# Performance work log

Hardware: AMD Instinct MI355X
Metric: run time of the kernel (lower is better)

Reference implementation:

```python
import jax, jax.numpy as jnp
import numpy as np

OUT, IN = 8192, 8192
GROUP = 128
N_GROUPS = IN // GROUP
BATCH = 64


def dequant_int4(packed, scales):
    # packed: [OUT, IN//2] int32 bytes in [0,256); two 4-bit codes per byte
    low = packed & 0xF            # first element of each pair
    high = (packed >> 4) & 0xF    # second element
    q = jnp.stack([low, high], axis=-1).reshape(OUT, IN)  # interleaved nibbles
    # symmetric grouped dequant: w = (q - 8) * scale, scale per [row, group]
    qg = q.reshape(OUT, N_GROUPS, GROUP).astype(scales.dtype)
    w = (qg - 8.0) * scales[:, :, None]
    return w.reshape(OUT, IN)


def setup_inputs() -> dict:
    key = jax.random.key(0)
    k1, k2, k3 = jax.random.split(key, 3)
    x = jax.random.normal(k1, (BATCH, IN), dtype=jnp.float32)
    packed = jax.random.randint(k2, (OUT, IN // 2), 0, 256, dtype=jnp.int32)
    scales = jax.random.uniform(k3, (OUT, N_GROUPS), dtype=jnp.float32)
    return {"x": x, "packed": packed, "scales": scales}


def reference(x, packed, scales):
    # Dequantize int4 weights then dense matmul (F.linear, no bias)
    w = dequant_int4(packed, scales)        # [OUT, IN]
    return jnp.einsum('bi,oi->bo', x, w)    # [BATCH, OUT]
```

## Files before the change

kernel.cpp:

```cpp
#include <hip/hip_runtime.h>
#include <hip/hip_bf16.h>
#include <stdint.h>

#define OUTN   8192
#define INN    8192
#define NGRP   64
#define BATCHN 64
#define BN     64
#define BK     128
#define KSPLIT 8
#define KCHUNK (INN / KSPLIT)
#define NITER  (KCHUNK / BK)
#define OSZ    (BATCHN * OUTN)

typedef __attribute__((ext_vector_type(8))) short bf16x8;
typedef __attribute__((ext_vector_type(4))) float f32x4;
typedef __attribute__((ext_vector_type(4))) unsigned int u32x4;

__device__ __forceinline__ unsigned short f2bf(float f) {
  __hip_bfloat16 h = __float2bfloat16(f);
  return __builtin_bit_cast(unsigned short, h);
}
__device__ __forceinline__ float bf2f(unsigned short h) {
  unsigned int u = ((unsigned int)h) << 16;
  return __builtin_bit_cast(float, u);
}

__global__ void qlin_prep(const float* __restrict__ x, float* __restrict__ xsum) {
  const int b = blockIdx.x;
  const int t = threadIdx.x;
  const float* xrow = x + (size_t)b * INN + t * 32;
  float s = 0.0f;
#pragma unroll
  for (int i = 0; i < 8; ++i) {
    float4 v = *(const float4*)(xrow + i * 4);
    s += bf2f(f2bf(v.x)) + bf2f(f2bf(v.y)) + bf2f(f2bf(v.z)) + bf2f(f2bf(v.w));
  }
  __shared__ float part[256];
  part[t] = s;
  __syncthreads();
  if (t < NGRP) {
    float g = part[4 * t] + part[4 * t + 1] + part[4 * t + 2] + part[4 * t + 3];
    xsum[t * BATCHN + b] = g;
  }
}

#define PKS 17
#define XTS 136

__global__ __launch_bounds__(256, 4) void qlin_main(
    const float* __restrict__ x, const int* __restrict__ packed,
    const float* __restrict__ scales, const float* __restrict__ xsum,
    float* __restrict__ out, float* __restrict__ part) {
  const int bx    = blockIdx.x;
  const int ks    = bx & (KSPLIT - 1);
  const int ntile = bx >> 3;
  const int o0    = ntile * BN;
  const int g0    = ks * NITER;

  const int t    = threadIdx.x;
  const int lane = t & 63;
  const int w    = t >> 6;
  const int l15  = lane & 15;
  const int quad = lane >> 4;

  __shared__ __align__(16) unsigned int   pk_c[BN * PKS];
  __shared__ __align__(16) unsigned short xt[BATCHN * XTS];
  __shared__ __align__(16) float          st[BN][9];
  __shared__ __align__(16) float          xs[NITER][BATCHN];

#pragma unroll
  for (int i = 0; i < 2; ++i) {
    int v = t * 2 + i;
    int ol = v >> 3, gl = v & 7;
    st[ol][gl] = scales[(size_t)(o0 + ol) * NGRP + g0 + gl];
    int gl2 = v >> 6, b2 = v & 63;
    xs[gl2][b2] = xsum[(g0 + gl2) * BATCHN + b2];
  }

  int4   pkr[4];
  float4 xr[8];

  const int prow = t >> 4, pcol = t & 15;
  const int xrow = t >> 5, xcol = t & 31;

  auto load_tile = [&](int i) {
    const int kk2 = ks * (KCHUNK / 2) + i * (BK / 2);
    const int* pbase = packed + (size_t)(o0 + prow) * (INN / 2) + kk2 + pcol * 4;
#pragma unroll
    for (int j = 0; j < 4; ++j)
      pkr[j] = *(const int4*)(pbase + (size_t)(16 * j) * (INN / 2));
    const int kk = ks * KCHUNK + i * BK;
    const float* xbase = x + (size_t)xrow * INN + kk + xcol * 4;
#pragma unroll
    for (int j = 0; j < 8; ++j)
      xr[j] = *(const float4*)(xbase + (size_t)(8 * j) * INN);
  };

  auto store_tile = [&]() {
#pragma unroll
    for (int j = 0; j < 4; ++j) {
      unsigned int c = (unsigned)pkr[j].x | ((unsigned)pkr[j].y << 8) |
                       ((unsigned)pkr[j].z << 16) | ((unsigned)pkr[j].w << 24);
      pk_c[(prow + 16 * j) * PKS + pcol] = c;
    }
#pragma unroll
    for (int j = 0; j < 8; ++j) {
      ushort4 h;
      h.x = f2bf(xr[j].x); h.y = f2bf(xr[j].y);
      h.z = f2bf(xr[j].z); h.w = f2bf(xr[j].w);
      *(ushort4*)&xt[(xrow + 8 * j) * XTS + xcol * 4] = h;
    }
  };

  f32x4 facc[4];
#pragma unroll
  for (int mt = 0; mt < 4; ++mt) facc[mt] = (f32x4){0.f, 0.f, 0.f, 0.f};

  load_tile(0);

  for (int i = 0; i < NITER; ++i) {
    __syncthreads();
    store_tile();
    if (i + 1 < NITER) load_tile(i + 1);
    __syncthreads();

    f32x4 gacc[4];
#pragma unroll
    for (int mt = 0; mt < 4; ++mt) gacc[mt] = (f32x4){0.f, 0.f, 0.f, 0.f};

#pragma unroll
    for (int kq = 0; kq < 4; ++kq) {
      bf16x8 af[4];
#pragma unroll
      for (int mt = 0; mt < 4; ++mt)
        af[mt] = *(const bf16x8*)&xt[(mt * 16 + l15) * XTS + kq * 32 + quad * 8];

      unsigned int c = pk_c[(w * 16 + l15) * PKS + kq * 4 + quad];
      u32x4 bw;
      bw.x = 0x43004300u | (c & 0xFu) | ((c & 0xF0u) << 12);
      bw.y = 0x43004300u | ((c >> 8) & 0xFu) | (((c >> 8) & 0xF0u) << 12);
      bw.z = 0x43004300u | ((c >> 16) & 0xFu) | (((c >> 16) & 0xF0u) << 12);
      bw.w = 0x43004300u | ((c >> 24) & 0xFu) | (((c >> 24) & 0xF0u) << 12);
      bf16x8 bfv = __builtin_bit_cast(bf16x8, bw);

#pragma unroll
      for (int mt = 0; mt < 4; ++mt)
        gacc[mt] = __builtin_amdgcn_mfma_f32_16x16x32_bf16(af[mt], bfv, gacc[mt], 0, 0, 0);
    }

    float s0 = st[w * 16 + l15][i];
#pragma unroll
    for (int mt = 0; mt < 4; ++mt) {
      f32x4 xv = *(const f32x4*)&xs[i][mt * 16 + quad * 4];
#pragma unroll
      for (int r = 0; r < 4; ++r)
        facc[mt][r] += s0 * (gacc[mt][r] - 136.0f * xv[r]);
    }
  }

  const int obase = o0 + w * 16 + l15;
  if (part) {
    float* pb = part + (size_t)ks * OSZ;
#pragma unroll
    for (int mt = 0; mt < 4; ++mt)
#pragma unroll
      for (int r = 0; r < 4; ++r) {
        int m = mt * 16 + quad * 4 + r;
        pb[(size_t)m * OUTN + obase] = facc[mt][r];
      }
  } else {
#pragma unroll
    for (int mt = 0; mt < 4; ++mt)
#pragma unroll
      for (int r = 0; r < 4; ++r) {
        int m = mt * 16 + quad * 4 + r;
        atomicAdd(&out[(size_t)m * OUTN + obase], facc[mt][r]);
      }
  }
}

__global__ void qlin_reduce(const float* __restrict__ part, float* __restrict__ out) {
  const size_t i = ((size_t)blockIdx.x * 256 + threadIdx.x) * 4;
  float4 s = *(const float4*)(part + i);
#pragma unroll
  for (int ks = 1; ks < KSPLIT; ++ks) {
    float4 v = *(const float4*)(part + (size_t)ks * OSZ + i);
    s.x += v.x; s.y += v.y; s.z += v.z; s.w += v.w;
  }
  *(float4*)(out + i) = s;
}

extern "C" void kernel_launch(void* const* d_in, const int* in_sizes, int n_in,
                              void* d_out, int out_size, void* d_ws, size_t ws_size,
                              hipStream_t stream) {
  const float* x      = (const float*)d_in[0];
  const int*   packed = (const int*)d_in[1];
  const float* scales = (const float*)d_in[2];
  float* out  = (float*)d_out;
  float* xsum = (float*)d_ws;
  const size_t part_off = 16384 / sizeof(float);
  const size_t need = 16384 + (size_t)KSPLIT * OSZ * sizeof(float);
  float* part = (ws_size >= need) ? ((float*)d_ws + part_off) : nullptr;

  qlin_prep<<<BATCHN, 256, 0, stream>>>(x, xsum);
  if (!part)
    hipMemsetAsync(d_out, 0, (size_t)out_size * sizeof(float), stream);
  qlin_main<<<(OUTN / BN) * KSPLIT, 256, 0, stream>>>(x, packed, scales, xsum, out, part);
  if (part)
    qlin_reduce<<<OSZ / 4 / 256, 256, 0, stream>>>(part, out);
}
```

Measured before the change: 207.5 us.

## Pre-convert activations to bf16 and stream tiles via direct global-to-LDS loads

The prep kernel now also writes a bf16 copy of x, so the main kernel loads half the activation bytes and skips per-tile conversion. Packed weights and bf16 activations go straight into double-buffered LDS through global_load_lds with an XOR swizzle, replacing the register staging and repacking of packed bytes. Tile K is halved, so there are two iterations per quant group, with the scale applied every other iteration. The cost is an extra bf16 buffer in workspace, and the packed int32 words are now read four bytes per nibble pair with no compaction.

```diff
diff --git a/kernel.cpp b/kernel.cpp
--- a/kernel.cpp
+++ b/kernel.cpp
@@ -7,13 +7,15 @@
 #define NGRP   64
 #define BATCHN 64
 #define BN     64
-#define BK     128
+#define BK     64
 #define KSPLIT 8
 #define KCHUNK (INN / KSPLIT)
 #define NITER  (KCHUNK / BK)
+#define NGRPC  (KCHUNK / 128)
 #define OSZ    (BATCHN * OUTN)
 
 typedef __attribute__((ext_vector_type(8))) short bf16x8;
+typedef __attribute__((ext_vector_type(8))) unsigned short u16x8;
 typedef __attribute__((ext_vector_type(4))) float f32x4;
 typedef __attribute__((ext_vector_type(4))) unsigned int u32x4;
 
@@ -26,37 +28,48 @@
   return __builtin_bit_cast(float, u);
 }
 
-__global__ void qlin_prep(const float* __restrict__ x, float* __restrict__ xsum) {
+__device__ __forceinline__ void gll16(const void* g, void* l) {
+  __builtin_amdgcn_global_load_lds(
+      (const __attribute__((address_space(1))) unsigned int*)g,
+      (__attribute__((address_space(3))) unsigned int*)l, 16, 0, 0);
+}
+
+__global__ void qlin_prep(const float* __restrict__ x, float* __restrict__ xsum,
+                          unsigned short* __restrict__ xbf) {
   const int b = blockIdx.x;
   const int t = threadIdx.x;
   const float* xrow = x + (size_t)b * INN + t * 32;
+  unsigned short* orow = xbf + (size_t)b * INN + t * 32;
   float s = 0.0f;
 #pragma unroll
-  for (int i = 0; i < 8; ++i) {
-    float4 v = *(const float4*)(xrow + i * 4);
-    s += bf2f(f2bf(v.x)) + bf2f(f2bf(v.y)) + bf2f(f2bf(v.z)) + bf2f(f2bf(v.w));
-  }
-  __shared__ float part[256];
-  part[t] = s;
+  for (int c = 0; c < 4; ++c) {
+    float4 v0 = *(const float4*)(xrow + c * 8);
+    float4 v1 = *(const float4*)(xrow + c * 8 + 4);
+    u16x8 h;
+    h[0] = f2bf(v0.x); h[1] = f2bf(v0.y); h[2] = f2bf(v0.z); h[3] = f2bf(v0.w);
+    h[4] = f2bf(v1.x); h[5] = f2bf(v1.y); h[6] = f2bf(v1.z); h[7] = f2bf(v1.w);
+#pragma unroll
+    for (int j = 0; j < 8; ++j) s += bf2f(h[j]);
+    *(u16x8*)(orow + c * 8) = h;
+  }
+  __shared__ float parts[256];
+  parts[t] = s;
   __syncthreads();
   if (t < NGRP) {
-    float g = part[4 * t] + part[4 * t + 1] + part[4 * t + 2] + part[4 * t + 3];
+    float g = parts[4 * t] + parts[4 * t + 1] + parts[4 * t + 2] + parts[4 * t + 3];
     xsum[t * BATCHN + b] = g;
   }
 }
 
-#define PKS 17
-#define XTS 136
-
 __global__ __launch_bounds__(256, 4) void qlin_main(
-    const float* __restrict__ x, const int* __restrict__ packed,
+    const int* __restrict__ packed, const unsigned short* __restrict__ xbf,
     const float* __restrict__ scales, const float* __restrict__ xsum,
     float* __restrict__ out, float* __restrict__ part) {
   const int bx    = blockIdx.x;
   const int ks    = bx & (KSPLIT - 1);
   const int ntile = bx >> 3;
   const int o0    = ntile * BN;
-  const int g0    = ks * NITER;
+  const int g0    = ks * NGRPC;
 
   const int t    = threadIdx.x;
   const int lane = t & 63;
@@ -64,10 +77,10 @@
   const int l15  = lane & 15;
   const int quad = lane >> 4;
 
-  __shared__ __align__(16) unsigned int   pk_c[BN * PKS];
-  __shared__ __align__(16) unsigned short xt[BATCHN * XTS];
-  __shared__ __align__(16) float          st[BN][9];
-  __shared__ __align__(16) float          xs[NITER][BATCHN];
+  __shared__ __align__(16) int4  pkb[2][512];
+  __shared__ __align__(16) int4  xb[2][512];
+  __shared__ __align__(16) float st[BN][9];
+  __shared__ __align__(16) float xs[NGRPC][BATCHN];
 
 #pragma unroll
   for (int i = 0; i < 2; ++i) {
@@ -78,88 +91,78 @@
     xs[gl2][b2] = xsum[(g0 + gl2) * BATCHN + b2];
   }
 
-  int4   pkr[4];
-  float4 xr[8];
-
-  const int prow = t >> 4, pcol = t & 15;
-  const int xrow = t >> 5, xcol = t & 31;
-
-  auto load_tile = [&](int i) {
-    const int kk2 = ks * (KCHUNK / 2) + i * (BK / 2);
-    const int* pbase = packed + (size_t)(o0 + prow) * (INN / 2) + kk2 + pcol * 4;
-#pragma unroll
-    for (int j = 0; j < 4; ++j)
-      pkr[j] = *(const int4*)(pbase + (size_t)(16 * j) * (INN / 2));
-    const int kk = ks * KCHUNK + i * BK;
-    const float* xbase = x + (size_t)xrow * INN + kk + xcol * 4;
-#pragma unroll
-    for (int j = 0; j < 8; ++j)
-      xr[j] = *(const float4*)(xbase + (size_t)(8 * j) * INN);
+  const int row0 = t >> 3;
+  const int p0   = t & 7;
+  const int c0   = p0 ^ (row0 & 7);
+  const char* pk0 = (const char*)packed + (size_t)(o0 + row0) * 16384 + ks * 2048 + c0 * 16;
+  const char* pk1 = pk0 + (size_t)32 * 16384;
+  const char* xg0 = (const char*)xbf + (size_t)row0 * 16384 + ks * 2048 + c0 * 16;
+  const char* xg1 = xg0 + (size_t)32 * 16384;
+
+  auto issue = [&](int i, int buf) {
+    const size_t off = (size_t)i * 128;
+    gll16(pk0 + off, &pkb[buf][t]);
+    gll16(pk1 + off, &pkb[buf][256 + t]);
+    gll16(xg0 + off, &xb[buf][t]);
+    gll16(xg1 + off, &xb[buf][256 + t]);
   };
 
-  auto store_tile = [&]() {
-#pragma unroll
-    for (int j = 0; j < 4; ++j) {
-      unsigned int c = (unsigned)pkr[j].x | ((unsigned)pkr[j].y << 8) |
-                       ((unsigned)pkr[j].z << 16) | ((unsigned)pkr[j].w << 24);
-      pk_c[(prow + 16 * j) * PKS + pcol] = c;
+  f32x4 facc[4], gacc[4];
+#pragma unroll
+  for (int mt = 0; mt < 4; ++mt) {
+    facc[mt] = (f32x4){0.f, 0.f, 0.f, 0.f};
+    gacc[mt] = (f32x4){0.f, 0.f, 0.f, 0.f};
+  }
+
+  issue(0, 0);
+  __syncthreads();
+
+  const int browB = w * 16 + l15;
+  const int sw    = l15 & 7;
+  int cur = 0;
+
+  for (int g = 0; g < NGRPC; ++g) {
+#pragma unroll
+    for (int h = 0; h < 2; ++h) {
+      const int i = g * 2 + h;
+      if (i + 1 < NITER) issue(i + 1, cur ^ 1);
+
+#pragma unroll
+      for (int kq = 0; kq < 2; ++kq) {
+        const int ch = kq * 4 + quad;
+        int4 v = pkb[cur][browB * 8 + (ch ^ sw)];
+        u32x4 bw;
+        bw.x = 0x43004300u | ((unsigned)v.x & 0xFu) | (((unsigned)v.x & 0xF0u) << 12);
+        bw.y = 0x43004300u | ((unsigned)v.y & 0xFu) | (((unsigned)v.y & 0xF0u) << 12);
+        bw.z = 0x43004300u | ((unsigned)v.z & 0xFu) | (((unsigned)v.z & 0xF0u) << 12);
+        bw.w = 0x43004300u | ((unsigned)v.w & 0xFu) | (((unsigned)v.w & 0xF0u) << 12);
+        bf16x8 bfv = __builtin_bit_cast(bf16x8, bw);
+#pragma unroll
+        for (int mt = 0; mt < 4; ++mt) {
+          bf16x8 af = *(const bf16x8*)&xb[cur][(mt * 16 + l15) * 8 + (ch ^ sw)];
+          gacc[mt] = __builtin_amdgcn_mfma_f32_16x16x32_bf16(af, bfv, gacc[mt], 0, 0, 0);
+        }
+      }
+
+      if (h == 1) {
+        float s0 = st[browB][g];
+#pragma unroll
+        for (int mt = 0; mt < 4; ++mt) {
+          f32x4 xv = *(const f32x4*)&xs[g][mt * 16 + quad * 4];
+#pragma unroll
+          for (int r = 0; r < 4; ++r) {
+            facc[mt][r] += s0 * (gacc[mt][r] - 136.0f * xv[r]);
+            gacc[mt][r] = 0.f;
+          }
+        }
+      }
+
+      __syncthreads();
+      cur ^= 1;
     }
-#pragma unroll
-    for (int j = 0; j < 8; ++j) {
-      ushort4 h;
-      h.x = f2bf(xr[j].x); h.y = f2bf(xr[j].y);
-      h.z = f2bf(xr[j].z); h.w = f2bf(xr[j].w);
-      *(ushort4*)&xt[(xrow + 8 * j) * XTS + xcol * 4] = h;
-    }
-  };
-
-  f32x4 facc[4];
-#pragma unroll
-  for (int mt = 0; mt < 4; ++mt) facc[mt] = (f32x4){0.f, 0.f, 0.f, 0.f};
-
-  load_tile(0);
-
-  for (int i = 0; i < NITER; ++i) {
-    __syncthreads();
-    store_tile();
-    if (i + 1 < NITER) load_tile(i + 1);
-    __syncthreads();
-
-    f32x4 gacc[4];
-#pragma unroll
-    for (int mt = 0; mt < 4; ++mt) gacc[mt] = (f32x4){0.f, 0.f, 0.f, 0.f};
-
-#pragma unroll
-    for (int kq = 0; kq < 4; ++kq) {
-      bf16x8 af[4];
-#pragma unroll
-      for (int mt = 0; mt < 4; ++mt)
-        af[mt] = *(const bf16x8*)&xt[(mt * 16 + l15) * XTS + kq * 32 + quad * 8];
-
-      unsigned int c = pk_c[(w * 16 + l15) * PKS + kq * 4 + quad];
-      u32x4 bw;
-      bw.x = 0x43004300u | (c & 0xFu) | ((c & 0xF0u) << 12);
-      bw.y = 0x43004300u | ((c >> 8) & 0xFu) | (((c >> 8) & 0xF0u) << 12);
-      bw.z = 0x43004300u | ((c >> 16) & 0xFu) | (((c >> 16) & 0xF0u) << 12);
-      bw.w = 0x43004300u | ((c >> 24) & 0xFu) | (((c >> 24) & 0xF0u) << 12);
-      bf16x8 bfv = __builtin_bit_cast(bf16x8, bw);
-
-#pragma unroll
-      for (int mt = 0; mt < 4; ++mt)
-        gacc[mt] = __builtin_amdgcn_mfma_f32_16x16x32_bf16(af[mt], bfv, gacc[mt], 0, 0, 0);
-    }
-
-    float s0 = st[w * 16 + l15][i];
-#pragma unroll
-    for (int mt = 0; mt < 4; ++mt) {
-      f32x4 xv = *(const f32x4*)&xs[i][mt * 16 + quad * 4];
-#pragma unroll
-      for (int r = 0; r < 4; ++r)
-        facc[mt][r] += s0 * (gacc[mt][r] - 136.0f * xv[r]);
-    }
-  }
-
-  const int obase = o0 + w * 16 + l15;
+  }
+
+  const int obase = o0 + browB;
   if (part) {
     float* pb = part + (size_t)ks * OSZ;
 #pragma unroll
@@ -198,15 +201,17 @@
   const int*   packed = (const int*)d_in[1];
   const float* scales = (const float*)d_in[2];
   float* out  = (float*)d_out;
-  float* xsum = (float*)d_ws;
-  const size_t part_off = 16384 / sizeof(float);
-  const size_t need = 16384 + (size_t)KSPLIT * OSZ * sizeof(float);
-  float* part = (ws_size >= need) ? ((float*)d_ws + part_off) : nullptr;
-
-  qlin_prep<<<BATCHN, 256, 0, stream>>>(x, xsum);
+
+  float*          xsum = (float*)d_ws;
+  unsigned short* xbf  = (unsigned short*)((char*)d_ws + 16384);
+  const size_t part_off = 16384 + (size_t)BATCHN * INN * 2;
+  const size_t need = part_off + (size_t)KSPLIT * OSZ * sizeof(float);
+  float* part = (ws_size >= need) ? (float*)((char*)d_ws + part_off) : nullptr;
+
+  qlin_prep<<<BATCHN, 256, 0, stream>>>(x, xsum, xbf);
   if (!part)
     hipMemsetAsync(d_out, 0, (size_t)out_size * sizeof(float), stream);
-  qlin_main<<<(OUTN / BN) * KSPLIT, 256, 0, stream>>>(x, packed, scales, xsum, out, part);
+  qlin_main<<<(OUTN / BN) * KSPLIT, 256, 0, stream>>>(packed, xbf, scales, xsum, out, part);
   if (part)
     qlin_reduce<<<OSZ / 4 / 256, 256, 0, stream>>>(part, out);
 }
```

Result: no change. 209.5 us (+1.0%).
